# Performance work log

Measured on AMD Instinct MI355X. Metric: run time of the kernel, lower is better.

Reference implementation:

```python
import jax, jax.numpy as jnp
import numpy as np

N_ENEMY = 4_000_000
N_GUN = 1_000_000
N_EDGES = 16_000_000
HID = 64
OUT = 8


def setup_inputs() -> dict:
    key = jax.random.key(0)
    ks = jax.random.split(key, 9)
    x_enemy = jax.random.normal(ks[0], (N_ENEMY, 4), dtype=jnp.float32)
    x_gun = jax.random.normal(ks[1], (N_GUN, 1), dtype=jnp.float32)
    edge_src = jax.random.randint(ks[2], (N_EDGES,), 0, N_ENEMY, dtype=jnp.int64 if jax.config.jax_enable_x64 else jnp.int32)
    edge_dst = jax.random.randint(ks[3], (N_EDGES,), 0, N_GUN, dtype=jnp.int64 if jax.config.jax_enable_x64 else jnp.int32)
    W_l = jax.random.normal(ks[4], (4, HID), dtype=jnp.float32) * 0.5
    b_l = jax.random.normal(ks[5], (HID,), dtype=jnp.float32) * 0.1
    W_r = jax.random.normal(ks[6], (1, HID), dtype=jnp.float32) * 0.5
    W_fc = jax.random.normal(ks[7], (HID, OUT), dtype=jnp.float32) * 0.1
    b_fc = jax.random.normal(ks[8], (OUT,), dtype=jnp.float32) * 0.1
    return {"x_enemy": x_enemy, "x_gun": x_gun, "edge_src": edge_src,
            "edge_dst": edge_dst, "W_l": W_l, "b_l": b_l, "W_r": W_r,
            "W_fc": W_fc, "b_fc": b_fc}


def reference(x_enemy, x_gun, edge_src, edge_dst, W_l, b_l, W_r, W_fc, b_fc):
    n_gun = x_gun.shape[0]
    # gather enemy messages along edges: [E, 4]
    msgs = x_enemy[edge_src]
    # mean aggregation per gun node (zero for isolated nodes, like PyG scatter-mean)
    summed = jax.ops.segment_sum(msgs, edge_dst, num_segments=n_gun)  # [N_gun, 4]
    counts = jax.ops.segment_sum(jnp.ones((edge_dst.shape[0],), dtype=x_enemy.dtype),
                                 edge_dst, num_segments=n_gun)       # [N_gun]
    mean = summed / jnp.maximum(counts, 1.0)[:, None]
    # SAGEConv: lin_l(aggr) + lin_r(x_dst)  (lin_l has bias, lin_r bias-free)
    h = mean @ W_l + b_l + x_gun @ W_r                                # [N_gun, HID]
    # linear head -> q values
    return h @ W_fc + b_fc                                            # [N_gun, OUT]
```

## Files before the change

kernel.cpp:

```cpp
#include <hip/hip_runtime.h>

#define N_ENEMY 4000000
#define N_GUN   1000000
#define N_EDGES 16000000
#define OUTD    8

#define NB   1024
#define GPB  977
#define T4   4096
#define NT4  3907
#define EPT4 16

#define CH   1024
#define CEPT 4

#define NS   8
#define SEG_CAP 16128

__device__ __forceinline__ unsigned int bucket_of(unsigned int dst) {
    return (unsigned int)(((unsigned long long)dst * 1125395730ull) >> 40);
}
__device__ __forceinline__ unsigned int rne_bf16(unsigned int u) {
    return (u + 0x7FFFu + ((u >> 16) & 1u)) >> 16;
}
__device__ __forceinline__ unsigned int get_xcc() {
    unsigned int x;
    asm("s_getreg_b32 %0, hwreg(HW_REG_XCC_ID)" : "=s"(x));
    return x;
}

__global__ void prep_params(const float* __restrict__ W_l, const float* __restrict__ b_l,
                            const float* __restrict__ W_r, const float* __restrict__ W_fc,
                            const float* __restrict__ b_fc, float* __restrict__ P) {
    int o = threadIdx.x;
    if (o < OUTD) {
        float a0 = 0.f, a1 = 0.f, a2 = 0.f, a3 = 0.f, r = 0.f, c = 0.f;
        for (int h = 0; h < 64; ++h) {
            float w = W_fc[h * OUTD + o];
            a0 += W_l[0 * 64 + h] * w;
            a1 += W_l[1 * 64 + h] * w;
            a2 += W_l[2 * 64 + h] * w;
            a3 += W_l[3 * 64 + h] * w;
            r  += W_r[h] * w;
            c  += b_l[h] * w;
        }
        P[0 * OUTD + o] = a0;
        P[1 * OUTD + o] = a1;
        P[2 * OUTD + o] = a2;
        P[3 * OUTD + o] = a3;
        P[4 * OUTD + o] = r;
        P[5 * OUTD + o] = c + b_fc[o];
    }
}

__global__ void conv_kernel(const uint4* __restrict__ xe, uint2* __restrict__ xeb) {
    int i = blockIdx.x * blockDim.x + threadIdx.x;
    if (i >= N_ENEMY) return;
    uint4 v = xe[i];
    uint2 q;
    q.x = rne_bf16(v.x) | (rne_bf16(v.y) << 16);
    q.y = rne_bf16(v.z) | (rne_bf16(v.w) << 16);
    xeb[i] = q;
}

__global__ void hist2_kernel(const int* __restrict__ edst, unsigned short* __restrict__ tileh) {
    __shared__ unsigned int lh[NB];
    int t = threadIdx.x;
    for (int i = t; i < NB; i += 256) lh[i] = 0;
    __syncthreads();
    int ebase = blockIdx.x * T4;
    int nE = N_EDGES - ebase;
    if (nE > T4) nE = T4;
    for (int i = t; i < nE; i += 256)
        atomicAdd(&lh[bucket_of((unsigned)edst[ebase + i])], 1u);
    __syncthreads();
    unsigned short* row = tileh + (size_t)blockIdx.x * NB;
    for (int i = t; i < NB; i += 256) row[i] = (unsigned short)lh[i];
}

template<int K>
__global__ __launch_bounds__(256)
void tile_scanT(unsigned short* __restrict__ tileh, unsigned int* __restrict__ tot,
                int nbk, int ntile) {
    __shared__ unsigned int part[256][17];
    int t = threadIdx.x;
    int b0 = blockIdx.x * 16;
    unsigned int loc[16];
#pragma unroll
    for (int j = 0; j < 16; ++j) loc[j] = 0;
    for (int k = 0; k < K; ++k) {
        int tile = t * K + k;
        if (tile < ntile) {
            const unsigned short* row = tileh + (size_t)tile * nbk + b0;
#pragma unroll
            for (int j = 0; j < 16; ++j) loc[j] += row[j];
        }
    }
#pragma unroll
    for (int j = 0; j < 16; ++j) part[t][j] = loc[j];
    __syncthreads();
    if (t < 16) {
        unsigned int acc = 0;
        for (int i = 0; i < 256; ++i) {
            unsigned int v = part[i][t];
            part[i][t] = acc;
            acc += v;
        }
        tot[b0 + t] = acc;
    }
    __syncthreads();
    unsigned int run[16];
#pragma unroll
    for (int j = 0; j < 16; ++j) run[j] = part[t][j];
    for (int k = 0; k < K; ++k) {
        int tile = t * K + k;
        if (tile < ntile) {
            unsigned short* row = tileh + (size_t)tile * nbk + b0;
#pragma unroll
            for (int j = 0; j < 16; ++j) {
                unsigned int c = row[j];
                row[j] = (unsigned short)run[j];
                run[j] += c;
            }
        }
    }
}

__global__ void scan_kernel(const unsigned int* __restrict__ tot,
                            unsigned int* __restrict__ offsets) {
    __shared__ unsigned int tmp[1024];
    int t = threadIdx.x;
    unsigned int v0 = (t < NB) ? tot[t] : 0u;
    tmp[t] = v0;
    __syncthreads();
    for (int d = 1; d < 1024; d <<= 1) {
        unsigned int v = (t >= d) ? tmp[t - d] : 0u;
        __syncthreads();
        tmp[t] += v;
        __syncthreads();
    }
    if (t < NB) offsets[t] = tmp[t] - v0;
    if (t == NB - 1) offsets[NB] = tmp[t];
}

__global__ __launch_bounds__(256, 4)
void scatter_sorted(const int* __restrict__ esrc, const int* __restrict__ edst,
                    const unsigned int* __restrict__ offsets,
                    const unsigned short* __restrict__ tileh,
                    unsigned int* __restrict__ payload) {
    __shared__ unsigned int cnt[NB];
    __shared__ unsigned int base[NB];
    __shared__ unsigned int gb[NB];
    __shared__ unsigned short bOf[T4];
    __shared__ unsigned int sorted[T4];
    __shared__ unsigned int partial[256];
    int t = threadIdx.x;
    int tile = blockIdx.x;
    int ebase = tile * T4;
    int nE = N_EDGES - ebase;
    if (nE > T4) nE = T4;
    for (int i = t; i < NB; i += 256) cnt[i] = 0;
    __syncthreads();
    unsigned int w[EPT4];
    unsigned int br[EPT4];
#pragma unroll
    for (int k = 0; k < EPT4; ++k) {
        int idx = k * 256 + t;
        if (idx < nE) {
            unsigned int s = (unsigned int)esrc[ebase + idx];
            unsigned int d = (unsigned int)edst[ebase + idx];
            unsigned int b = bucket_of(d);
            unsigned int g = d - b * GPB;
            unsigned int r = atomicAdd(&cnt[b], 1u);
            w[k]  = (s << 10) | g;
            br[k] = (b << 13) | r;
        } else br[k] = 0xFFFFFFFFu;
    }
    __syncthreads();
    unsigned int loc[4];
    unsigned int s = 0;
#pragma unroll
    for (int j = 0; j < 4; ++j) {
        int b = t * 4 + j;
        unsigned int c = cnt[b];
        loc[j] = s; s += c;
    }
    partial[t] = s;
    __syncthreads();
    for (int d = 1; d < 256; d <<= 1) {
        unsigned int v = (t >= d) ? partial[t - d] : 0u;
        __syncthreads();
        partial[t] += v;
        __syncthreads();
    }
    unsigned int excl = (t > 0) ? partial[t - 1] : 0u;
#pragma unroll
    for (int j = 0; j < 4; ++j) base[t * 4 + j] = excl + loc[j];
    __syncthreads();
    const unsigned short* trow = tileh + (size_t)tile * NB;
#pragma unroll
    for (int j = 0; j < 4; ++j) {
        int b = t * 4 + j;
        gb[b] = offsets[b] + (unsigned int)trow[b];
        unsigned int bs = base[b];
        unsigned int c = cnt[b];
        for (unsigned int p = bs; p < bs + c; ++p) bOf[p] = (unsigned short)b;
    }
    __syncthreads();
#pragma unroll
    for (int k = 0; k < EPT4; ++k) {
        if (br[k] != 0xFFFFFFFFu) {
            unsigned int b = br[k] >> 13;
            unsigned int r = br[k] & 8191u;
            sorted[base[b] + r] = w[k];
        }
    }
    __syncthreads();
    for (int p = t; p < nE; p += 256) {
        unsigned int b = bOf[p];
        payload[gb[b] + ((unsigned int)p - base[b])] = sorted[p];
    }
}

__global__ __launch_bounds__(256)
void slice_sort(const unsigned int* __restrict__ offsets,
                unsigned int* __restrict__ payload,
                unsigned int* __restrict__ stab) {
    __shared__ unsigned int A[SEG_CAP];
    __shared__ unsigned int cnt[NS];
    __shared__ unsigned int base[NS + 1];
    int b = blockIdx.x;
    int t = threadIdx.x;
    unsigned int segS = offsets[b];
    unsigned int segE = offsets[b + 1];
    unsigned int len = segE - segS;
    if (len > SEG_CAP) {
        if (t <= NS) stab[b * (NS + 1) + t] = (t == 0) ? segS : segE;
        return;
    }
    if (t < NS) cnt[t] = 0;
    __syncthreads();
    for (unsigned int i = t; i < len; i += 256) {
        unsigned int w = payload[segS + i];
        A[i] = w;
        atomicAdd(&cnt[w >> 29], 1u);
    }
    __syncthreads();
    if (t == 0) {
        unsigned int acc = 0;
        for (int k = 0; k < NS; ++k) { base[k] = acc; acc += cnt[k]; }
        base[NS] = acc;
    }
    __syncthreads();
    if (t < NS) cnt[t] = 0;
    __syncthreads();
    for (unsigned int i = t; i < len; i += 256) {
        unsigned int w = A[i];
        unsigned int k = w >> 29;
        unsigned int r = atomicAdd(&cnt[k], 1u);
        payload[segS + base[k] + r] = w;
    }
    if (t <= NS) stab[b * (NS + 1) + t] = segS + base[t];
}

__global__ __launch_bounds__(256)
void bucket_v9(const unsigned int* __restrict__ stab,
               const unsigned int* __restrict__ payload,
               const uint2* __restrict__ xeb,
               const float* __restrict__ xg,
               const float* __restrict__ P,
               float* __restrict__ out) {
    __shared__ unsigned long long sorted[CH];
    __shared__ unsigned int cnt[1024];
    __shared__ unsigned int base_[1024];
    __shared__ unsigned int partial[256];
    __shared__ float sP[48];
    int t = threadIdx.x;
    if (t < 48) sP[t] = P[t];
    __syncthreads();

    float a0[4] = {0,0,0,0}, a1[4] = {0,0,0,0}, a2[4] = {0,0,0,0}, a3[4] = {0,0,0,0};
    float an[4] = {0,0,0,0};

    unsigned int b = blockIdx.x;
    unsigned int rot = get_xcc() & (NS - 1u);

    for (int si = 0; si < NS; ++si) {
        unsigned int s = ((unsigned int)si + rot) & (NS - 1u);
        unsigned int rs = stab[b * (NS + 1) + s];
        unsigned int re = stab[b * (NS + 1) + s + 1];

        for (unsigned int cs = rs; cs < re; cs += CH) {
            int n = (int)((re - cs < (unsigned int)CH) ? (re - cs) : (unsigned int)CH);
            for (int i = t; i < 1024; i += 256) cnt[i] = 0;
            __syncthreads();

            unsigned int g_[CEPT], r_[CEPT];
            uint2 q_[CEPT];
#pragma unroll
            for (int k = 0; k < CEPT; ++k) {
                int idx = k * 256 + t;
                if (idx < n) {
                    unsigned int p = payload[cs + idx];
                    q_[k] = xeb[p >> 10];
                    unsigned int g = p & 1023u;
                    g_[k] = g;
                    r_[k] = atomicAdd(&cnt[g], 1u);
                } else g_[k] = 0xFFFFFFFFu;
            }
            __syncthreads();

            unsigned int myc[4];
            unsigned int loc[4];
            unsigned int acc = 0;
#pragma unroll
            for (int j = 0; j < 4; ++j) {
                myc[j] = cnt[t * 4 + j];
                loc[j] = acc; acc += myc[j];
            }
            partial[t] = acc;
            __syncthreads();
            for (int d = 1; d < 256; d <<= 1) {
                unsigned int v = (t >= d) ? partial[t - d] : 0u;
                __syncthreads();
                partial[t] += v;
                __syncthreads();
            }
            unsigned int excl = (t > 0) ? partial[t - 1] : 0u;
            unsigned int myb[4];
#pragma unroll
            for (int j = 0; j < 4; ++j) {
                myb[j] = excl + loc[j];
                base_[t * 4 + j] = myb[j];
            }
            __syncthreads();

#pragma unroll
            for (int k = 0; k < CEPT; ++k) {
                if (g_[k] != 0xFFFFFFFFu) {
                    sorted[base_[g_[k]] + r_[k]] =
                        ((unsigned long long)q_[k].y << 32) | (unsigned long long)q_[k].x;
                }
            }
            __syncthreads();

#pragma unroll
            for (int j = 0; j < 4; ++j) {
                unsigned int bs = myb[j], c = myc[j];
                for (unsigned int p2 = bs; p2 < bs + c; ++p2) {
                    unsigned long long v = sorted[p2];
                    unsigned int lo = (unsigned int)v, hi = (unsigned int)(v >> 32);
                    a0[j] += __uint_as_float(lo << 16);
                    a1[j] += __uint_as_float(lo & 0xffff0000u);
                    a2[j] += __uint_as_float(hi << 16);
                    a3[j] += __uint_as_float(hi & 0xffff0000u);
                }
                an[j] += (float)c;
            }
            __syncthreads();
        }
    }

#pragma unroll
    for (int j = 0; j < 4; ++j) {
        int g = t * 4 + j;
        if (g >= GPB) continue;
        unsigned int G = b * GPB + (unsigned int)g;
        if (G >= N_GUN) continue;
        float inv = 1.0f / fmaxf(an[j], 1.0f);
        float m0 = a0[j] * inv, m1 = a1[j] * inv, m2 = a2[j] * inv, m3 = a3[j] * inv;
        float xv = xg[G];
        float res[OUTD];
#pragma unroll
        for (int o = 0; o < OUTD; ++o) {
            res[o] = m0 * sP[o] + m1 * sP[8 + o] + m2 * sP[16 + o] + m3 * sP[24 + o]
                   + xv * sP[32 + o] + sP[40 + o];
        }
        float4* op = (float4*)(out + (size_t)G * OUTD);
        op[0] = make_float4(res[0], res[1], res[2], res[3]);
        op[1] = make_float4(res[4], res[5], res[6], res[7]);
    }
}

__global__ void edge_kernel(const int4* __restrict__ esrc4, const int4* __restrict__ edst4,
                            const float4* __restrict__ xe, float* __restrict__ summed,
                            float* __restrict__ counts) {
    int t = blockIdx.x * blockDim.x + threadIdx.x;
    if (t >= N_EDGES / 4) return;
    int4 s4 = esrc4[t];
    int4 d4 = edst4[t];
    int ss[4] = { s4.x, s4.y, s4.z, s4.w };
    int dd[4] = { d4.x, d4.y, d4.z, d4.w };
#pragma unroll
    for (int k = 0; k < 4; ++k) {
        float4 m = xe[ss[k]];
        float* basep = summed + (size_t)dd[k] * 4;
        atomicAdd(basep + 0, m.x);
        atomicAdd(basep + 1, m.y);
        atomicAdd(basep + 2, m.z);
        atomicAdd(basep + 3, m.w);
        atomicAdd(counts + dd[k], 1.0f);
    }
}

__global__ void gun_kernel(const float4* __restrict__ summed, const float* __restrict__ counts,
                           const float* __restrict__ xg, const float* __restrict__ P,
                           float* __restrict__ out) {
    __shared__ float sP[48];
    if (threadIdx.x < 48) sP[threadIdx.x] = P[threadIdx.x];
    __syncthreads();
    int g = blockIdx.x * blockDim.x + threadIdx.x;
    if (g >= N_GUN) return;
    float4 s = summed[g];
    float cnt = counts[g];
    float inv = 1.0f / fmaxf(cnt, 1.0f);
    float m0 = s.x * inv, m1 = s.y * inv, m2 = s.z * inv, m3 = s.w * inv;
    float xv = xg[g];
    float res[OUTD];
#pragma unroll
    for (int o = 0; o < OUTD; ++o) {
        res[o] = m0 * sP[o] + m1 * sP[8 + o] + m2 * sP[16 + o] + m3 * sP[24 + o]
               + xv * sP[32 + o] + sP[40 + o];
    }
    float4* op = (float4*)(out + (size_t)g * OUTD);
    op[0] = make_float4(res[0], res[1], res[2], res[3]);
    op[1] = make_float4(res[4], res[5], res[6], res[7]);
}

extern "C" void kernel_launch(void* const* d_in, const int* in_sizes, int n_in,
                              void* d_out, int out_size, void* d_ws, size_t ws_size,
                              hipStream_t stream) {
    const float* x_enemy = (const float*)d_in[0];
    const float* x_gun   = (const float*)d_in[1];
    const int*   esrc    = (const int*)d_in[2];
    const int*   edst    = (const int*)d_in[3];
    const float* W_l     = (const float*)d_in[4];
    const float* b_l     = (const float*)d_in[5];
    const float* W_r     = (const float*)d_in[6];
    const float* W_fc    = (const float*)d_in[7];
    const float* b_fc    = (const float*)d_in[8];
    float* out = (float*)d_out;

    const size_t PAYLOAD_OFF = 0;
    const size_t XEB_OFF     = (size_t)N_EDGES;
    const size_t TOT_OFF     = XEB_OFF + (size_t)N_ENEMY*2;
    const size_t OFFS_OFF    = TOT_OFF + NB;
    const size_t P_OFF       = OFFS_OFF + NB + 1;
    const size_t STAB_OFF    = P_OFF + 48;
    const size_t NEEDED_FULL = (STAB_OFF + (size_t)NB * (NS + 1) + 16) * sizeof(unsigned int);

    if (ws_size >= NEEDED_FULL) {
        unsigned int*   ws      = (unsigned int*)d_ws;
        unsigned int*   payload = ws + PAYLOAD_OFF;
        uint2*          xeb     = (uint2*)(ws + XEB_OFF);
        unsigned short* tileh   = (unsigned short*)(ws + XEB_OFF);
        unsigned int*   tot     = ws + TOT_OFF;
        unsigned int*   offsets = ws + OFFS_OFF;
        float*          P       = (float*)(ws + P_OFF);
        unsigned int*   stab    = ws + STAB_OFF;

        prep_params<<<1, 64, 0, stream>>>(W_l, b_l, W_r, W_fc, b_fc, P);
        hist2_kernel<<<NT4, 256, 0, stream>>>(edst, tileh);
        tile_scanT<16><<<NB / 16, 256, 0, stream>>>(tileh, tot, NB, NT4);
        scan_kernel<<<1, 1024, 0, stream>>>(tot, offsets);
        scatter_sorted<<<NT4, 256, 0, stream>>>(esrc, edst, offsets, tileh, payload);
        slice_sort<<<NB, 256, 0, stream>>>(offsets, payload, stab);
        conv_kernel<<<(N_ENEMY + 255) / 256, 256, 0, stream>>>((const uint4*)x_enemy, xeb);
        bucket_v9<<<NB, 256, 0, stream>>>(stab, payload, xeb, x_gun, P, out);
    } else {
        float* summed = (float*)d_ws;
        float* counts = summed + (size_t)N_GUN * 4;
        float* P      = counts + N_GUN;
        hipMemsetAsync(d_ws, 0, ((size_t)N_GUN * 5 + 48) * sizeof(float), stream);
        prep_params<<<1, 64, 0, stream>>>(W_l, b_l, W_r, W_fc, b_fc, P);
        int edge_threads = N_EDGES / 4;
        edge_kernel<<<(edge_threads + 255) / 256, 256, 0, stream>>>(
            (const int4*)esrc, (const int4*)edst, (const float4*)x_enemy, summed, counts);
        gun_kernel<<<(N_GUN + 255) / 256, 256, 0, stream>>>(
            (const float4*)summed, counts, x_gun, P, out);
    }
}
```

Before: 376.7 us.

## Use 2048 power-of-two dst buckets with shift-based bucketing

Raises the number of destination buckets from 1024 to 2048, each covering 512 gun nodes, and replaces the multiply-shift bucket function with a plain shift and mask. The scan kernel, scatter, slice sort (now radix on bits 28+) and bucket accumulation are all adjusted to the new bucket width. Each thread now accumulates 2 gun nodes instead of 4, and twice as many blocks run the final stage. Scatter launch bounds drop to 3 blocks per SM because the shared arrays doubled, which may reduce occupancy. Smaller buckets give less work per block and cheaper indexing, at the cost of larger per-tile histograms (more hist/tileh traffic) and more scatter shared memory.

```diff
diff --git a/kernel.cpp b/kernel.cpp
--- a/kernel.cpp
+++ b/kernel.cpp
@@ -5,8 +5,9 @@
 #define N_EDGES 16000000
 #define OUTD    8
 
-#define NB   1024
-#define GPB  977
+#define NB   2048
+#define GSH  9
+#define GPB  512
 #define T4   4096
 #define NT4  3907
 #define EPT4 16
@@ -15,11 +16,8 @@
 #define CEPT 4
 
 #define NS   8
-#define SEG_CAP 16128
-
-__device__ __forceinline__ unsigned int bucket_of(unsigned int dst) {
-    return (unsigned int)(((unsigned long long)dst * 1125395730ull) >> 40);
-}
+#define SEG_CAP 10240
+
 __device__ __forceinline__ unsigned int rne_bf16(unsigned int u) {
     return (u + 0x7FFFu + ((u >> 16) & 1u)) >> 16;
 }
@@ -72,7 +70,7 @@
     int nE = N_EDGES - ebase;
     if (nE > T4) nE = T4;
     for (int i = t; i < nE; i += 256)
-        atomicAdd(&lh[bucket_of((unsigned)edst[ebase + i])], 1u);
+        atomicAdd(&lh[((unsigned)edst[ebase + i]) >> GSH], 1u);
     __syncthreads();
     unsigned short* row = tileh + (size_t)blockIdx.x * NB;
     for (int i = t; i < NB; i += 256) row[i] = (unsigned short)lh[i];
@@ -126,12 +124,13 @@
     }
 }
 
-__global__ void scan_kernel(const unsigned int* __restrict__ tot,
-                            unsigned int* __restrict__ offsets) {
+__global__ void scan2048(const unsigned int* __restrict__ tot,
+                         unsigned int* __restrict__ offs) {
     __shared__ unsigned int tmp[1024];
     int t = threadIdx.x;
-    unsigned int v0 = (t < NB) ? tot[t] : 0u;
-    tmp[t] = v0;
+    unsigned int a = tot[2 * t], b = tot[2 * t + 1];
+    unsigned int p = a + b;
+    tmp[t] = p;
     __syncthreads();
     for (int d = 1; d < 1024; d <<= 1) {
         unsigned int v = (t >= d) ? tmp[t - d] : 0u;
@@ -139,11 +138,13 @@
         tmp[t] += v;
         __syncthreads();
     }
-    if (t < NB) offsets[t] = tmp[t] - v0;
-    if (t == NB - 1) offsets[NB] = tmp[t];
-}
-
-__global__ __launch_bounds__(256, 4)
+    unsigned int excl = tmp[t] - p;
+    offs[2 * t] = excl;
+    offs[2 * t + 1] = excl + a;
+    if (t == 1023) offs[2048] = tmp[t];
+}
+
+__global__ __launch_bounds__(256, 3)
 void scatter_sorted(const int* __restrict__ esrc, const int* __restrict__ edst,
                     const unsigned int* __restrict__ offsets,
                     const unsigned short* __restrict__ tileh,
@@ -169,19 +170,19 @@
         if (idx < nE) {
             unsigned int s = (unsigned int)esrc[ebase + idx];
             unsigned int d = (unsigned int)edst[ebase + idx];
-            unsigned int b = bucket_of(d);
-            unsigned int g = d - b * GPB;
+            unsigned int b = d >> GSH;
+            unsigned int g = d & (GPB - 1u);
             unsigned int r = atomicAdd(&cnt[b], 1u);
-            w[k]  = (s << 10) | g;
+            w[k]  = (s << GSH) | g;
             br[k] = (b << 13) | r;
         } else br[k] = 0xFFFFFFFFu;
     }
     __syncthreads();
-    unsigned int loc[4];
+    unsigned int loc[8];
     unsigned int s = 0;
 #pragma unroll
-    for (int j = 0; j < 4; ++j) {
-        int b = t * 4 + j;
+    for (int j = 0; j < 8; ++j) {
+        int b = t * 8 + j;
         unsigned int c = cnt[b];
         loc[j] = s; s += c;
     }
@@ -195,12 +196,12 @@
     }
     unsigned int excl = (t > 0) ? partial[t - 1] : 0u;
 #pragma unroll
-    for (int j = 0; j < 4; ++j) base[t * 4 + j] = excl + loc[j];
+    for (int j = 0; j < 8; ++j) base[t * 8 + j] = excl + loc[j];
     __syncthreads();
     const unsigned short* trow = tileh + (size_t)tile * NB;
 #pragma unroll
-    for (int j = 0; j < 4; ++j) {
-        int b = t * 4 + j;
+    for (int j = 0; j < 8; ++j) {
+        int b = t * 8 + j;
         gb[b] = offsets[b] + (unsigned int)trow[b];
         unsigned int bs = base[b];
         unsigned int c = cnt[b];
@@ -243,7 +244,7 @@
     for (unsigned int i = t; i < len; i += 256) {
         unsigned int w = payload[segS + i];
         A[i] = w;
-        atomicAdd(&cnt[w >> 29], 1u);
+        atomicAdd(&cnt[w >> 28], 1u);
     }
     __syncthreads();
     if (t == 0) {
@@ -256,7 +257,7 @@
     __syncthreads();
     for (unsigned int i = t; i < len; i += 256) {
         unsigned int w = A[i];
-        unsigned int k = w >> 29;
+        unsigned int k = w >> 28;
         unsigned int r = atomicAdd(&cnt[k], 1u);
         payload[segS + base[k] + r] = w;
     }
@@ -271,16 +272,16 @@
                const float* __restrict__ P,
                float* __restrict__ out) {
     __shared__ unsigned long long sorted[CH];
-    __shared__ unsigned int cnt[1024];
-    __shared__ unsigned int base_[1024];
+    __shared__ unsigned int cnt[GPB];
+    __shared__ unsigned int base_[GPB];
     __shared__ unsigned int partial[256];
     __shared__ float sP[48];
     int t = threadIdx.x;
     if (t < 48) sP[t] = P[t];
     __syncthreads();
 
-    float a0[4] = {0,0,0,0}, a1[4] = {0,0,0,0}, a2[4] = {0,0,0,0}, a3[4] = {0,0,0,0};
-    float an[4] = {0,0,0,0};
+    float a0[2] = {0,0}, a1[2] = {0,0}, a2[2] = {0,0}, a3[2] = {0,0};
+    float an[2] = {0,0};
 
     unsigned int b = blockIdx.x;
     unsigned int rot = get_xcc() & (NS - 1u);
@@ -292,7 +293,7 @@
 
         for (unsigned int cs = rs; cs < re; cs += CH) {
             int n = (int)((re - cs < (unsigned int)CH) ? (re - cs) : (unsigned int)CH);
-            for (int i = t; i < 1024; i += 256) cnt[i] = 0;
+            for (int i = t; i < GPB; i += 256) cnt[i] = 0;
             __syncthreads();
 
             unsigned int g_[CEPT], r_[CEPT];
@@ -302,20 +303,20 @@
                 int idx = k * 256 + t;
                 if (idx < n) {
                     unsigned int p = payload[cs + idx];
-                    q_[k] = xeb[p >> 10];
-                    unsigned int g = p & 1023u;
+                    q_[k] = xeb[p >> GSH];
+                    unsigned int g = p & (GPB - 1u);
                     g_[k] = g;
                     r_[k] = atomicAdd(&cnt[g], 1u);
                 } else g_[k] = 0xFFFFFFFFu;
             }
             __syncthreads();
 
-            unsigned int myc[4];
-            unsigned int loc[4];
+            unsigned int myc[2];
+            unsigned int loc[2];
             unsigned int acc = 0;
 #pragma unroll
-            for (int j = 0; j < 4; ++j) {
-                myc[j] = cnt[t * 4 + j];
+            for (int j = 0; j < 2; ++j) {
+                myc[j] = cnt[t * 2 + j];
                 loc[j] = acc; acc += myc[j];
             }
             partial[t] = acc;
@@ -327,11 +328,11 @@
                 __syncthreads();
             }
             unsigned int excl = (t > 0) ? partial[t - 1] : 0u;
-            unsigned int myb[4];
-#pragma unroll
-            for (int j = 0; j < 4; ++j) {
+            unsigned int myb[2];
+#pragma unroll
+            for (int j = 0; j < 2; ++j) {
                 myb[j] = excl + loc[j];
-                base_[t * 4 + j] = myb[j];
+                base_[t * 2 + j] = myb[j];
             }
             __syncthreads();
 
@@ -345,7 +346,7 @@
             __syncthreads();
 
 #pragma unroll
-            for (int j = 0; j < 4; ++j) {
+            for (int j = 0; j < 2; ++j) {
                 unsigned int bs = myb[j], c = myc[j];
                 for (unsigned int p2 = bs; p2 < bs + c; ++p2) {
                     unsigned long long v = sorted[p2];
@@ -362,10 +363,9 @@
     }
 
 #pragma unroll
-    for (int j = 0; j < 4; ++j) {
-        int g = t * 4 + j;
-        if (g >= GPB) continue;
-        unsigned int G = b * GPB + (unsigned int)g;
+    for (int j = 0; j < 2; ++j) {
+        int g = t * 2 + j;
+        unsigned int G = (b << GSH) + (unsigned int)g;
         if (G >= N_GUN) continue;
         float inv = 1.0f / fmaxf(an[j], 1.0f);
         float m0 = a0[j] * inv, m1 = a1[j] * inv, m2 = a2[j] * inv, m3 = a3[j] * inv;
@@ -462,7 +462,7 @@
         prep_params<<<1, 64, 0, stream>>>(W_l, b_l, W_r, W_fc, b_fc, P);
         hist2_kernel<<<NT4, 256, 0, stream>>>(edst, tileh);
         tile_scanT<16><<<NB / 16, 256, 0, stream>>>(tileh, tot, NB, NT4);
-        scan_kernel<<<1, 1024, 0, stream>>>(tot, offsets);
+        scan2048<<<1, 1024, 0, stream>>>(tot, offsets);
         scatter_sorted<<<NT4, 256, 0, stream>>>(esrc, edst, offsets, tileh, payload);
         slice_sort<<<NB, 256, 0, stream>>>(offsets, payload, stab);
         conv_kernel<<<(N_ENEMY + 255) / 256, 256, 0, stream>>>((const uint4*)x_enemy, xeb);
```

Result: slower. 514.7 us (+36.6%).

## Split each bucket's gather-reduce across two blocks with a separate combine kernel

Applied to the files above, without the earlier changes.

The final bucket kernel now launches two blocks per bucket, each handling alternating 1024-edge chunks. Each block writes per-gun partial sums, rounded to bf16, plus a 16-bit count to workspace. A new kernel adds the two partials and applies the mean and the fused linear layers. This doubles the grid from 1024 to 2048 blocks to fill more CUs, at the cost of an extra launch, extra global traffic, and extra bf16 rounding of the partial sums, which could hurt accuracy.

```diff
diff --git a/kernel.cpp b/kernel.cpp
--- a/kernel.cpp
+++ b/kernel.cpp
@@ -264,6 +264,152 @@
 }
 
 __global__ __launch_bounds__(256)
+void bucket_v9s(const unsigned int* __restrict__ stab,
+                const unsigned int* __restrict__ payload,
+                const uint2* __restrict__ xeb,
+                unsigned long long* __restrict__ sumP,
+                unsigned short* __restrict__ cntP) {
+    __shared__ unsigned long long sorted[CH];
+    __shared__ unsigned int cnt[1024];
+    __shared__ unsigned int base_[1024];
+    __shared__ unsigned int partial[256];
+    int t = threadIdx.x;
+
+    float a0[4] = {0,0,0,0}, a1[4] = {0,0,0,0}, a2[4] = {0,0,0,0}, a3[4] = {0,0,0,0};
+    float an[4] = {0,0,0,0};
+
+    unsigned int b    = (unsigned int)blockIdx.x >> 1;
+    unsigned int half = (unsigned int)blockIdx.x & 1u;
+    unsigned int rot = get_xcc() & (NS - 1u);
+
+    for (int si = 0; si < NS; ++si) {
+        unsigned int s = ((unsigned int)si + rot) & (NS - 1u);
+        unsigned int rs = stab[b * (NS + 1) + s];
+        unsigned int re = stab[b * (NS + 1) + s + 1];
+
+        for (unsigned int cs = rs + half * CH; cs < re; cs += 2u * CH) {
+            int n = (int)((re - cs < (unsigned int)CH) ? (re - cs) : (unsigned int)CH);
+            for (int i = t; i < 1024; i += 256) cnt[i] = 0;
+            __syncthreads();
+
+            unsigned int g_[CEPT], r_[CEPT];
+            uint2 q_[CEPT];
+#pragma unroll
+            for (int k = 0; k < CEPT; ++k) {
+                int idx = k * 256 + t;
+                if (idx < n) {
+                    unsigned int p = payload[cs + idx];
+                    q_[k] = xeb[p >> 10];
+                    unsigned int g = p & 1023u;
+                    g_[k] = g;
+                    r_[k] = atomicAdd(&cnt[g], 1u);
+                } else g_[k] = 0xFFFFFFFFu;
+            }
+            __syncthreads();
+
+            unsigned int myc[4];
+            unsigned int loc[4];
+            unsigned int acc = 0;
+#pragma unroll
+            for (int j = 0; j < 4; ++j) {
+                myc[j] = cnt[t * 4 + j];
+                loc[j] = acc; acc += myc[j];
+            }
+            partial[t] = acc;
+            __syncthreads();
+            for (int d = 1; d < 256; d <<= 1) {
+                unsigned int v = (t >= d) ? partial[t - d] : 0u;
+                __syncthreads();
+                partial[t] += v;
+                __syncthreads();
+            }
+            unsigned int excl = (t > 0) ? partial[t - 1] : 0u;
+            unsigned int myb[4];
+#pragma unroll
+            for (int j = 0; j < 4; ++j) {
+                myb[j] = excl + loc[j];
+                base_[t * 4 + j] = myb[j];
+            }
+            __syncthreads();
+
+#pragma unroll
+            for (int k = 0; k < CEPT; ++k) {
+                if (g_[k] != 0xFFFFFFFFu) {
+                    sorted[base_[g_[k]] + r_[k]] =
+                        ((unsigned long long)q_[k].y << 32) | (unsigned long long)q_[k].x;
+                }
+            }
+            __syncthreads();
+
+#pragma unroll
+            for (int j = 0; j < 4; ++j) {
+                unsigned int bs = myb[j], c = myc[j];
+                for (unsigned int p2 = bs; p2 < bs + c; ++p2) {
+                    unsigned long long v = sorted[p2];
+                    unsigned int lo = (unsigned int)v, hi = (unsigned int)(v >> 32);
+                    a0[j] += __uint_as_float(lo << 16);
+                    a1[j] += __uint_as_float(lo & 0xffff0000u);
+                    a2[j] += __uint_as_float(hi << 16);
+                    a3[j] += __uint_as_float(hi & 0xffff0000u);
+                }
+                an[j] += (float)c;
+            }
+            __syncthreads();
+        }
+    }
+
+    size_t pb = (size_t)blockIdx.x * GPB;
+#pragma unroll
+    for (int j = 0; j < 4; ++j) {
+        int g = t * 4 + j;
+        if (g >= GPB) continue;
+        unsigned long long lo = (unsigned long long)(rne_bf16(__float_as_uint(a0[j])) |
+                                                    (rne_bf16(__float_as_uint(a1[j])) << 16));
+        unsigned long long hi = (unsigned long long)(rne_bf16(__float_as_uint(a2[j])) |
+                                                    (rne_bf16(__float_as_uint(a3[j])) << 16));
+        sumP[pb + g] = lo | (hi << 32);
+        cntP[pb + g] = (unsigned short)an[j];
+    }
+}
+
+__global__ void gun_final2(const unsigned long long* __restrict__ sumP,
+                           const unsigned short* __restrict__ cntP,
+                           const float* __restrict__ xg, const float* __restrict__ P,
+                           float* __restrict__ out) {
+    __shared__ float sP[48];
+    if (threadIdx.x < 48) sP[threadIdx.x] = P[threadIdx.x];
+    __syncthreads();
+    int G = blockIdx.x * blockDim.x + threadIdx.x;
+    if (G >= N_GUN) return;
+    unsigned int b = bucket_of((unsigned)G);
+    unsigned int g = (unsigned)G - b * GPB;
+    size_t i0 = (size_t)(2 * b) * GPB + g;
+    size_t i1 = (size_t)(2 * b + 1) * GPB + g;
+    unsigned long long v0 = sumP[i0], v1 = sumP[i1];
+    float cnt = (float)cntP[i0] + (float)cntP[i1];
+    float m0 = __uint_as_float(((unsigned int)v0 & 0xffffu) << 16)
+             + __uint_as_float(((unsigned int)v1 & 0xffffu) << 16);
+    float m1 = __uint_as_float((unsigned int)v0 & 0xffff0000u)
+             + __uint_as_float((unsigned int)v1 & 0xffff0000u);
+    float m2 = __uint_as_float(((unsigned int)(v0 >> 32) & 0xffffu) << 16)
+             + __uint_as_float(((unsigned int)(v1 >> 32) & 0xffffu) << 16);
+    float m3 = __uint_as_float((unsigned int)(v0 >> 32) & 0xffff0000u)
+             + __uint_as_float((unsigned int)(v1 >> 32) & 0xffff0000u);
+    float inv = 1.0f / fmaxf(cnt, 1.0f);
+    m0 *= inv; m1 *= inv; m2 *= inv; m3 *= inv;
+    float xv = xg[G];
+    float res[OUTD];
+#pragma unroll
+    for (int o = 0; o < OUTD; ++o) {
+        res[o] = m0 * sP[o] + m1 * sP[8 + o] + m2 * sP[16 + o] + m3 * sP[24 + o]
+               + xv * sP[32 + o] + sP[40 + o];
+    }
+    float4* op = (float4*)(out + (size_t)G * OUTD);
+    op[0] = make_float4(res[0], res[1], res[2], res[3]);
+    op[1] = make_float4(res[4], res[5], res[6], res[7]);
+}
+
+__global__ __launch_bounds__(256)
 void bucket_v9(const unsigned int* __restrict__ stab,
                const unsigned int* __restrict__ payload,
                const uint2* __restrict__ xeb,
@@ -278,23 +424,18 @@
     int t = threadIdx.x;
     if (t < 48) sP[t] = P[t];
     __syncthreads();
-
     float a0[4] = {0,0,0,0}, a1[4] = {0,0,0,0}, a2[4] = {0,0,0,0}, a3[4] = {0,0,0,0};
     float an[4] = {0,0,0,0};
-
     unsigned int b = blockIdx.x;
     unsigned int rot = get_xcc() & (NS - 1u);
-
     for (int si = 0; si < NS; ++si) {
         unsigned int s = ((unsigned int)si + rot) & (NS - 1u);
         unsigned int rs = stab[b * (NS + 1) + s];
         unsigned int re = stab[b * (NS + 1) + s + 1];
-
         for (unsigned int cs = rs; cs < re; cs += CH) {
             int n = (int)((re - cs < (unsigned int)CH) ? (re - cs) : (unsigned int)CH);
             for (int i = t; i < 1024; i += 256) cnt[i] = 0;
             __syncthreads();
-
             unsigned int g_[CEPT], r_[CEPT];
             uint2 q_[CEPT];
 #pragma unroll
@@ -309,7 +450,6 @@
                 } else g_[k] = 0xFFFFFFFFu;
             }
             __syncthreads();
-
             unsigned int myc[4];
             unsigned int loc[4];
             unsigned int acc = 0;
@@ -334,7 +474,6 @@
                 base_[t * 4 + j] = myb[j];
             }
             __syncthreads();
-
 #pragma unroll
             for (int k = 0; k < CEPT; ++k) {
                 if (g_[k] != 0xFFFFFFFFu) {
@@ -343,7 +482,6 @@
                 }
             }
             __syncthreads();
-
 #pragma unroll
             for (int j = 0; j < 4; ++j) {
                 unsigned int bs = myb[j], c = myc[j];
@@ -360,7 +498,6 @@
             __syncthreads();
         }
     }
-
 #pragma unroll
     for (int j = 0; j < 4; ++j) {
         int g = t * 4 + j;
@@ -447,9 +584,14 @@
     const size_t OFFS_OFF    = TOT_OFF + NB;
     const size_t P_OFF       = OFFS_OFF + NB + 1;
     const size_t STAB_OFF    = P_OFF + 48;
-    const size_t NEEDED_FULL = (STAB_OFF + (size_t)NB * (NS + 1) + 16) * sizeof(unsigned int);
-
-    if (ws_size >= NEEDED_FULL) {
+    const size_t END17       = STAB_OFF + (size_t)NB * (NS + 1) + 16;
+    const size_t SUMP_OFF    = (END17 + 1) & ~(size_t)1;
+    const size_t CNTP_OFF    = SUMP_OFF + (size_t)2 * NB * GPB * 2;
+    const size_t END_SPLIT   = CNTP_OFF + ((size_t)2 * NB * GPB + 1) / 2;
+    const size_t NEEDED_17   = END17 * sizeof(unsigned int);
+    const size_t NEEDED_SPL  = END_SPLIT * sizeof(unsigned int);
+
+    if (ws_size >= NEEDED_17) {
         unsigned int*   ws      = (unsigned int*)d_ws;
         unsigned int*   payload = ws + PAYLOAD_OFF;
         uint2*          xeb     = (uint2*)(ws + XEB_OFF);
@@ -466,7 +608,15 @@
         scatter_sorted<<<NT4, 256, 0, stream>>>(esrc, edst, offsets, tileh, payload);
         slice_sort<<<NB, 256, 0, stream>>>(offsets, payload, stab);
         conv_kernel<<<(N_ENEMY + 255) / 256, 256, 0, stream>>>((const uint4*)x_enemy, xeb);
-        bucket_v9<<<NB, 256, 0, stream>>>(stab, payload, xeb, x_gun, P, out);
+
+        if (ws_size >= NEEDED_SPL) {
+            unsigned long long* sumP = (unsigned long long*)(ws + SUMP_OFF);
+            unsigned short*     cntP = (unsigned short*)(ws + CNTP_OFF);
+            bucket_v9s<<<NB * 2, 256, 0, stream>>>(stab, payload, xeb, sumP, cntP);
+            gun_final2<<<(N_GUN + 255) / 256, 256, 0, stream>>>(sumP, cntP, x_gun, P, out);
+        } else {
+            bucket_v9<<<NB, 256, 0, stream>>>(stab, payload, xeb, x_gun, P, out);
+        }
     } else {
         float* summed = (float*)d_ws;
         float* counts = summed + (size_t)N_GUN * 4;
```

Measured after the change: 461.8 us. 1.23x slower.
